# Performance work log

Measured on AMD Instinct MI355X. Metric: run time of the kernel, lower is better.

Reference implementation:

```python
import jax, jax.numpy as jnp
import numpy as np

N_HEADS = 16
DIM = 1024
HEAD_DIM = DIM // N_HEADS

def setup_inputs() -> dict:
    key = jax.random.key(0)
    ks = jax.random.split(key, 5)
    x = jax.random.normal(ks[0], (4, 2048, DIM), dtype=jnp.float32)
    W_attn = jax.random.normal(ks[1], (DIM, 3 * DIM), dtype=jnp.float32) / np.sqrt(DIM)
    b_attn = jnp.zeros((3 * DIM,), dtype=jnp.float32)
    W_proj = jax.random.normal(ks[2], (DIM, DIM), dtype=jnp.float32) / np.sqrt(DIM)
    b_proj = jnp.zeros((DIM,), dtype=jnp.float32)
    return {"x": x, "W_attn": W_attn, "b_attn": b_attn, "W_proj": W_proj, "b_proj": b_proj}

def reference(x, W_attn, b_attn, W_proj, b_proj):
    B, S, D = x.shape
    qkv = x @ W_attn + b_attn                      # [B,S,3D]
    q, k, v = jnp.split(qkv, 3, axis=2)
    def heads(t):
        return t.reshape(B, S, N_HEADS, HEAD_DIM).transpose(0, 2, 1, 3)  # [B,H,S,hd]
    qh, kh, vh = heads(q), heads(k), heads(v)
    scale = 1.0 / np.sqrt(HEAD_DIM).astype(np.float32)
    scores = jnp.einsum('bhqd,bhkd->bhqk', qh, kh) * scale  # [B,H,S,S]
    causal = jnp.tril(jnp.ones((S, S), dtype=bool))
    scores = jnp.where(causal, scores, -jnp.inf)
    probs = jax.nn.softmax(scores, axis=-1)
    ctx = jnp.einsum('bhqk,bhkd->bhqd', probs, vh)           # [B,H,S,hd]
    ctx = ctx.transpose(0, 2, 1, 3).reshape(B, S, D)
    return ctx @ W_proj + b_proj
```

## Files before the change

### kernel.cpp

```cpp
#include <hip/hip_runtime.h>
#include <hip/hip_bf16.h>
#include <stdint.h>

typedef __attribute__((ext_vector_type(4))) float  f32x4a;
typedef __attribute__((ext_vector_type(8))) short  bf16x8s;
typedef __attribute__((ext_vector_type(8))) unsigned short u16x8;

#define QSCALE 0.18033688011112042f

static __device__ __forceinline__ unsigned short f2bf(float f) {
    union { float f; uint32_t u; } v; v.f = f;
    uint32_t u = v.u;
    return (unsigned short)((u + 0x7FFFu + ((u >> 16) & 1u)) >> 16);
}

static __device__ __forceinline__ unsigned int pack2bf(float lo, float hi) {
    __hip_bfloat162 t = __float22bfloat162_rn(make_float2(lo, hi));
    union { __hip_bfloat162 b; unsigned int u; } c; c.b = t;
    return c.u;
}

static __device__ __forceinline__ float exp2a(float x) {
    float r;
    asm("v_exp_f32 %0, %1" : "=v"(r) : "v"(x));
    return r;
}

#define GLL(src, dst)                                                          \
    __builtin_amdgcn_global_load_lds(                                          \
        (const __attribute__((address_space(1))) void*)(src),                  \
        (__attribute__((address_space(3))) void*)(dst), 16, 0, 0)

__global__ __launch_bounds__(256) void k_cvt_bf16(const float* __restrict__ in,
                                                  unsigned short* __restrict__ out, int n8) {
    int i = blockIdx.x * blockDim.x + threadIdx.x;
    if (i >= n8) return;
    const float4* p = (const float4*)(in + (size_t)i * 8);
    float4 a = p[0], b = p[1];
    u16x8 o;
    o[0] = f2bf(a.x); o[1] = f2bf(a.y); o[2] = f2bf(a.z); o[3] = f2bf(a.w);
    o[4] = f2bf(b.x); o[5] = f2bf(b.y); o[6] = f2bf(b.z); o[7] = f2bf(b.w);
    *(u16x8*)(out + (size_t)i * 8) = o;
}

__global__ __launch_bounds__(256) void k_scale_bias(const float* __restrict__ b,
                                                    float* __restrict__ out,
                                                    int n, int nscale, float sc) {
    int i = blockIdx.x * blockDim.x + threadIdx.x;
    if (i >= n) return;
    out[i] = b[i] * (i < nscale ? sc : 1.0f);
}

__global__ __launch_bounds__(256) void k_transpose_w(const float* __restrict__ W,
                                                     unsigned short* __restrict__ Wt,
                                                     int K, int N, float sc, int nscale) {
    __shared__ float tile[64][68];
    int bx = blockIdx.x;
    int ntn = N >> 6;
    int kt = bx / ntn, nt = bx % ntn;
    int t = threadIdx.x;
    int r0 = t >> 4;
    int c4 = (t & 15) << 2;
    for (int i = 0; i < 4; ++i) {
        int k = r0 + i * 16;
        float4 v = *(const float4*)(W + (size_t)(kt * 64 + k) * N + nt * 64 + c4);
        tile[k][c4 + 0] = v.x; tile[k][c4 + 1] = v.y;
        tile[k][c4 + 2] = v.z; tile[k][c4 + 3] = v.w;
    }
    __syncthreads();
    int nl = t >> 2;
    int kc = (t & 3) << 4;
    float s = (nt * 64 + nl < nscale) ? sc : 1.0f;
    unsigned short* dst = Wt + (size_t)(nt * 64 + nl) * K + kt * 64 + kc;
    u16x8 o0, o1;
    for (int i = 0; i < 8; ++i) o0[i] = f2bf(tile[kc + i][nl] * s);
    for (int i = 0; i < 8; ++i) o1[i] = f2bf(tile[kc + 8 + i][nl] * s);
    *(u16x8*)dst = o0;
    *(u16x8*)(dst + 8) = o1;
}

template<int OUT_BF16, int VW>
__global__ __launch_bounds__(512, 2) void k_gemm8p(const unsigned short* __restrict__ A,
                                                   const unsigned short* __restrict__ Bt,
                                                   const float* __restrict__ bias,
                                                   void* __restrict__ Cout,
                                                   unsigned short* __restrict__ vt,
                                                   int M, int N, int K, int ntn) {
    __shared__ __align__(16) unsigned short S[8][8192];
    unsigned short* Sb = &S[0][0];

    int nwg = gridDim.x;
    int bid = blockIdx.x;
    int wg = (bid & 7) * (nwg >> 3) + (bid >> 3);
    int mt = wg / ntn, nt = wg % ntn;
    size_t m0 = (size_t)mt * 256, n0 = (size_t)nt * 256;

    int tid = threadIdx.x;
    int w = tid >> 6, lane = tid & 63;
    int wm = w >> 2, wn = w & 3;
    int l15 = lane & 15, l4 = lane >> 4;

    int srow = tid >> 2;
    int sc = (tid & 3) ^ ((srow >> 1) & 3);
    const unsigned short* Asrc = A  + (m0 + srow) * (size_t)K + sc * 8;
    const unsigned short* Bsrc = Bt + (n0 + srow) * (size_t)K + sc * 8;

#define SLOT(buf, arr, kh) ((((buf) << 2) | ((arr) << 1) | (kh)) * 8192)
#define STAGE(buf, arr, kh, kt)                                                           \
    do {                                                                                  \
        const unsigned short* s_ = ((arr) ? Bsrc : Asrc) + (size_t)(kt) * 64 + (kh) * 32; \
        GLL(s_,                    Sb + SLOT(buf, arr, kh) + tid * 8);                    \
        GLL(s_ + (size_t)128 * K,  Sb + SLOT(buf, arr, kh) + 4096 + tid * 8);             \
    } while (0)

    int ck = (l4 ^ ((l15 >> 1) & 3)) * 8;
    int arowb = wm * 128 + l15;
    int browb = wn * 64 + l15;

#define LD_AF(dst, buf, kh, mh)                                                           \
    _Pragma("unroll")                                                                     \
    for (int q = 0; q < 4; ++q)                                                           \
        dst[q] = *(const bf16x8s*)(Sb + SLOT(buf, 0, kh) + (arowb + (mh) * 64 + q * 16) * 32 + ck);
#define LD_BF(dst, buf, kh)                                                               \
    _Pragma("unroll")                                                                     \
    for (int q = 0; q < 4; ++q)                                                           \
        dst[q] = *(const bf16x8s*)(Sb + SLOT(buf, 1, kh) + (browb + q * 16) * 32 + ck);

    f32x4a acc[8][4] = {};

#define MFMA16(mh, afv, bfv)                                                              \
    do {                                                                                  \
        __builtin_amdgcn_s_setprio(1);                                                    \
        _Pragma("unroll")                                                                 \
        for (int mf = 0; mf < 4; ++mf)                                                    \
            _Pragma("unroll")                                                             \
            for (int nf = 0; nf < 4; ++nf)                                                \
                acc[(mh) * 4 + mf][nf] = __builtin_amdgcn_mfma_f32_16x16x32_bf16(         \
                    afv[mf], bfv[nf], acc[(mh) * 4 + mf][nf], 0, 0, 0);                   \
        __builtin_amdgcn_s_setprio(0);                                                    \
    } while (0)

#define BAR() __builtin_amdgcn_s_barrier()
#define LGKM0()                                                                           \
    do {                                                                                  \
        asm volatile("s_waitcnt lgkmcnt(0)" ::: "memory");                                \
        __builtin_amdgcn_sched_barrier(0);                                                \
    } while (0)

    int NT = K >> 6;

    STAGE(0, 1, 0, 0);
    STAGE(0, 0, 0, 0);
    STAGE(0, 1, 1, 0);
    STAGE(0, 0, 1, 0);
    STAGE(1, 1, 0, 1);
    STAGE(1, 0, 0, 1);
    STAGE(1, 1, 1, 1);
    asm volatile("s_waitcnt vmcnt(6)" ::: "memory");
    __builtin_amdgcn_sched_barrier(0);
    BAR();

    bf16x8s af[4], bf[4], bf2[4];
    for (int t0 = 0; t0 < NT; t0 += 2) {
        int t1 = t0 + 1;
        bool more = (t0 + 2) < NT;
        LD_AF(af, 0, 0, 0);  LD_BF(bf, 0, 0);
        STAGE(1, 0, 1, t1);
        BAR(); LGKM0();
        MFMA16(0, af, bf);
        BAR();
        LD_AF(af, 0, 0, 1);
        if (more) STAGE(0, 1, 0, t0 + 2);
        BAR(); LGKM0();
        MFMA16(1, af, bf);
        BAR();
        LD_AF(af, 0, 1, 0);  LD_BF(bf2, 0, 1);
        if (more) STAGE(0, 0, 0, t0 + 2);
        BAR(); LGKM0();
        MFMA16(0, af, bf2);
        BAR();
        LD_AF(af, 0, 1, 1);
        if (more) STAGE(0, 1, 1, t0 + 2);
        BAR(); LGKM0();
        MFMA16(1, af, bf2);
        if (more) { asm volatile("s_waitcnt vmcnt(6)" ::: "memory"); }
        else      { asm volatile("s_waitcnt vmcnt(0)" ::: "memory"); }
        __builtin_amdgcn_sched_barrier(0);
        BAR();
        LD_AF(af, 1, 0, 0);  LD_BF(bf, 1, 0);
        if (more) STAGE(0, 0, 1, t0 + 2);
        BAR(); LGKM0();
        MFMA16(0, af, bf);
        BAR();
        LD_AF(af, 1, 0, 1);
        if (more) STAGE(1, 1, 0, t1 + 2);
        BAR(); LGKM0();
        MFMA16(1, af, bf);
        BAR();
        LD_AF(af, 1, 1, 0);  LD_BF(bf2, 1, 1);
        if (more) STAGE(1, 0, 0, t1 + 2);
        BAR(); LGKM0();
        MFMA16(0, af, bf2);
        BAR();
        LD_AF(af, 1, 1, 1);
        if (more) STAGE(1, 1, 1, t1 + 2);
        BAR(); LGKM0();
        MFMA16(1, af, bf2);
        if (more) {
            asm volatile("s_waitcnt vmcnt(6)" ::: "memory");
            __builtin_amdgcn_sched_barrier(0);
        }
        BAR();
    }

    if (VW && nt >= 8) {
        int b = (int)(m0 >> 11);
        int sbase = ((int)m0 & 2047) + wm * 128;
        #pragma unroll
        for (int nf = 0; nf < 4; ++nf) {
            int vc = ((int)n0 - 2048) + wn * 64 + nf * 16 + l15;
            int h = vc >> 6, d = vc & 63;
            float bv = bias[2048 + vc];
            unsigned short* vrow = vt + ((size_t)(b * 16 + h) * 64 + d) * 2048;
            #pragma unroll
            for (int mf = 0; mf < 8; ++mf) {
                int s = sbase + mf * 16 + l4 * 4;
                uint2 pv = make_uint2(pack2bf(acc[mf][nf][0] + bv, acc[mf][nf][1] + bv),
                                      pack2bf(acc[mf][nf][2] + bv, acc[mf][nf][3] + bv));
                *(uint2*)(vrow + s) = pv;
            }
        }
    } else {
        #pragma unroll
        for (int nf = 0; nf < 4; ++nf) {
            int col = (int)n0 + wn * 64 + nf * 16 + l15;
            float bv = bias[col];
            #pragma unroll
            for (int mf = 0; mf < 8; ++mf) {
                int rbase = (int)m0 + wm * 128 + mf * 16 + l4 * 4;
                #pragma unroll
                for (int rr = 0; rr < 4; ++rr) {
                    float v = acc[mf][nf][rr] + bv;
                    if (OUT_BF16)
                        ((unsigned short*)Cout)[(size_t)(rbase + rr) * N + col] = f2bf(v);
                    else
                        ((float*)Cout)[(size_t)(rbase + rr) * N + col] = v;
                }
            }
        }
    }
#undef SLOT
#undef STAGE
#undef LD_AF
#undef LD_BF
#undef MFMA16
#undef BAR
#undef LGKM0
}

__global__ __launch_bounds__(256, 4) void k_attn(const unsigned short* __restrict__ qkv,
                                                 const unsigned short* __restrict__ vt,
                                                 unsigned short* __restrict__ ctx) {
    __shared__ unsigned short Ks[2][4096];
    __shared__ unsigned short Vs[2][4096];
    __shared__ unsigned short Pb[4][1024];
    int bx = blockIdx.x;
    int bh = bx & 63;
    int pr = bx >> 6;
    int b = bh >> 4, hd = bh & 15;
    int tid = threadIdx.x;
    int w = tid >> 6, lane = tid & 63;
    int l15 = lane & 15, l4 = lane >> 4;

    const unsigned short* Qb  = qkv + (size_t)b * 2048 * 3072 + hd * 64;
    const unsigned short* Kb  = Qb + 1024;
    const unsigned short* Vtb = vt + (size_t)bh * 64 * 2048;

    int kr0 = tid >> 3, kc0 = tid & 7;
    int kr1 = (tid + 256) >> 3, kc1 = tid & 7;
    const unsigned short* Ksr0 = Kb  + (size_t)kr0 * 3072 + ((kc0 ^ (kr0 & 7)) << 3);
    const unsigned short* Ksr1 = Kb  + (size_t)kr1 * 3072 + ((kc1 ^ (kr1 & 7)) << 3);
    const unsigned short* Vsr0 = Vtb + (size_t)kr0 * 2048 + ((kc0 ^ (kr0 & 7)) << 3);
    const unsigned short* Vsr1 = Vtb + (size_t)kr1 * 2048 + ((kc1 ^ (kr1 & 7)) << 3);
    unsigned short* pbw = &Pb[w][0];

    int prow = l15 * 64;
    int psw  = l15 & 7;
    int ph   = (l4 & 1) * 4;
    int pc0  = ((0 + (l4 >> 1)) ^ psw) * 8;
    int pc1  = ((2 + (l4 >> 1)) ^ psw) * 8;
    int pc2  = ((4 + (l4 >> 1)) ^ psw) * 8;
    int pc3  = ((6 + (l4 >> 1)) ^ psw) * 8;
    int pr0  = ((0 + l4) ^ psw) * 8;
    int pr1  = ((4 + l4) ^ psw) * 8;

#define STAGE(buf, kv0s)                                                                        \
    do {                                                                                        \
        size_t ko_ = (size_t)(kv0s) * 3072;                                                     \
        GLL(Ksr0 + ko_,     &Ks[buf][w * 512]);                                                 \
        GLL(Ksr1 + ko_,     &Ks[buf][2048 + w * 512]);                                          \
        GLL(Vsr0 + (kv0s),  &Vs[buf][w * 512]);                                                 \
        GLL(Vsr1 + (kv0s),  &Vs[buf][2048 + w * 512]);                                          \
    } while (0)

    for (int half = 0; half < 2; ++half) {
        int j = half ? (31 - pr) : pr;
        int q0 = j * 64 + w * 16;
        int qa = q0 + l15;
        bf16x8s qf0, qf1;
        {
            const unsigned short* p = Qb + (size_t)(q0 + l15) * 3072 + l4 * 8;
            qf0 = *(const bf16x8s*)p;
            qf1 = *(const bf16x8s*)(p + 32);
        }
        f32x4a o[4] = {};
        float lrow = 0.0f;
        const int NSTEPS = j + 1;

        STAGE(0, 0);
        __syncthreads();

        int s = 0;
        while (true) {
            int cur = s & 1;
            int kv0 = s << 6;
            if (s + 1 < NSTEPS) STAGE(cur ^ 1, kv0 + 64);

            const unsigned short* Kbuf = Ks[cur];
            const unsigned short* Vbuf = Vs[cur];

            f32x4a z[4];
            __builtin_amdgcn_s_setprio(1);
            #pragma unroll
            for (int f = 0; f < 4; ++f) {
                int rk = f * 16 + l15;
                bf16x8s ka = *(const bf16x8s*)(Kbuf + rk * 64 + ((l4 ^ psw) << 3));
                bf16x8s kb = *(const bf16x8s*)(Kbuf + rk * 64 + (((4 + l4) ^ psw) << 3));
                f32x4a zz = {0.f, 0.f, 0.f, 0.f};
                zz = __builtin_amdgcn_mfma_f32_16x16x32_bf16(ka, qf0, zz, 0, 0, 0);
                zz = __builtin_amdgcn_mfma_f32_16x16x32_bf16(kb, qf1, zz, 0, 0, 0);
                z[f] = zz;
            }
            __builtin_amdgcn_s_setprio(0);

            bf16x8s vf[2][4];
            #pragma unroll
            for (int g = 0; g < 2; ++g)
                #pragma unroll
                for (int nf = 0; nf < 4; ++nf) {
                    int rv = nf * 16 + l15;
                    vf[g][nf] = *(const bf16x8s*)(Vbuf + rv * 64 + (((g * 4 + l4) ^ (rv & 7)) << 3));
                }

            if (s == NSTEPS - 1) {
                #pragma unroll
                for (int f = 0; f < 4; ++f)
                    #pragma unroll
                    for (int r = 0; r < 4; ++r)
                        if (kv0 + f * 16 + l4 * 4 + r > qa) z[f][r] = -1e30f;
            }

            f32x4a p4[4];
            #pragma unroll
            for (int f = 0; f < 4; ++f)
                #pragma unroll
                for (int r = 0; r < 4; ++r)
                    p4[f][r] = exp2a(z[f][r]);

            f32x4a ps = (p4[0] + p4[1]) + (p4[2] + p4[3]);
            float psum = (ps[0] + ps[1]) + (ps[2] + ps[3]);
            psum += __shfl_xor(psum, 16);
            psum += __shfl_xor(psum, 32);
            lrow += psum;

            unsigned int pk[8];
            #pragma unroll
            for (int f = 0; f < 4; ++f) {
                pk[2 * f]     = pack2bf(p4[f][0], p4[f][1]);
                pk[2 * f + 1] = pack2bf(p4[f][2], p4[f][3]);
            }

            *(uint2*)(pbw + prow + pc0 + ph) = make_uint2(pk[0], pk[1]);
            *(uint2*)(pbw + prow + pc1 + ph) = make_uint2(pk[2], pk[3]);
            *(uint2*)(pbw + prow + pc2 + ph) = make_uint2(pk[4], pk[5]);
            *(uint2*)(pbw + prow + pc3 + ph) = make_uint2(pk[6], pk[7]);
            asm volatile("" ::: "memory");
            bf16x8s pa0 = *(const bf16x8s*)(pbw + prow + pr0);
            bf16x8s pa1 = *(const bf16x8s*)(pbw + prow + pr1);
            asm volatile("" ::: "memory");

            __builtin_amdgcn_s_setprio(1);
            #pragma unroll
            for (int nf = 0; nf < 4; ++nf)
                o[nf] = __builtin_amdgcn_mfma_f32_16x16x32_bf16(pa0, vf[0][nf], o[nf], 0, 0, 0);
            #pragma unroll
            for (int nf = 0; nf < 4; ++nf)
                o[nf] = __builtin_amdgcn_mfma_f32_16x16x32_bf16(pa1, vf[1][nf], o[nf], 0, 0, 0);
            __builtin_amdgcn_s_setprio(0);

            ++s;
            if (s == NSTEPS) break;
            __syncthreads();
        }
        __syncthreads();

        float linv[4];
        #pragma unroll
        for (int r = 0; r < 4; ++r) linv[r] = 1.0f / __shfl(lrow, l4 * 4 + r);
        #pragma unroll
        for (int nf = 0; nf < 4; ++nf) {
            int col = hd * 64 + nf * 16 + l15;
            #pragma unroll
            for (int r = 0; r < 4; ++r) {
                int row = q0 + l4 * 4 + r;
                ctx[((size_t)b * 2048 + row) * 1024 + col] = f2bf(o[nf][r] * linv[r]);
            }
        }
    }
#undef STAGE
}

extern "C" void kernel_launch(void* const* d_in, const int* in_sizes, int n_in,
                              void* d_out, int out_size, void* d_ws, size_t ws_size,
                              hipStream_t stream) {
    const float* x      = (const float*)d_in[0];
    const float* W_attn = (const float*)d_in[1];
    const float* b_attn = (const float*)d_in[2];
    const float* W_proj = (const float*)d_in[3];
    const float* b_proj = (const float*)d_in[4];

    char* ws = (char*)d_ws;
    unsigned short* xb  = (unsigned short*)ws; ws += (size_t)8192 * 1024 * 2;
    unsigned short* wta = (unsigned short*)ws; ws += (size_t)3072 * 1024 * 2;
    unsigned short* wtp = (unsigned short*)ws; ws += (size_t)1024 * 1024 * 2;
    unsigned short* qkv = (unsigned short*)ws; ws += (size_t)8192 * 3072 * 2;
    unsigned short* vt  = (unsigned short*)ws; ws += (size_t)64 * 64 * 2048 * 2;
    unsigned short* ctx = (unsigned short*)ws; ws += (size_t)8192 * 1024 * 2;
    float*          sbias = (float*)ws;

    k_cvt_bf16<<<4096, 256, 0, stream>>>(x, xb, 8192 * 1024 / 8);
    k_transpose_w<<<16 * 48, 256, 0, stream>>>(W_attn, wta, 1024, 3072, QSCALE, 1024);
    k_transpose_w<<<16 * 16, 256, 0, stream>>>(W_proj, wtp, 1024, 1024, 1.0f, 0);
    k_scale_bias<<<12, 256, 0, stream>>>(b_attn, sbias, 3072, 1024, QSCALE);
    k_gemm8p<1, 1><<<384, 512, 0, stream>>>(xb, wta, sbias, (void*)qkv, vt, 8192, 3072, 1024, 12);
    k_attn<<<1024, 256, 0, stream>>>(qkv, vt, ctx);
    k_gemm8p<0, 0><<<128, 512, 0, stream>>>(ctx, wtp, b_proj, d_out, nullptr, 8192, 1024, 1024, 4);
}
```

Before: 182.5 us.

## Switch GEMMs to 128x256 tiles with triple-buffered 64-wide K stages

Replaces the 256x256-tile double-buffered GEMM with a 128x256 tile whose K=64 slices sit in a three-slot LDS ring with an 8-chunk XOR swizzle. The grid doubles (768 and 256 workgroups), which gives more waves per CU and better fill across the GPU, especially for the small projection GEMM. Each workgroup now reuses A less per B load and has fewer MFMAs per barrier. LDS use changes to 3*(16K+32K) bytes, which may limit how many workgroups fit per CU.

```diff
diff --git a/kernel.cpp b/kernel.cpp
--- a/kernel.cpp
+++ b/kernel.cpp
@@ -80,63 +80,68 @@
 }
 
 template<int OUT_BF16, int VW>
-__global__ __launch_bounds__(512, 2) void k_gemm8p(const unsigned short* __restrict__ A,
+__global__ __launch_bounds__(512, 2) void k_gemm3b(const unsigned short* __restrict__ A,
                                                    const unsigned short* __restrict__ Bt,
                                                    const float* __restrict__ bias,
                                                    void* __restrict__ Cout,
                                                    unsigned short* __restrict__ vt,
                                                    int M, int N, int K, int ntn) {
-    __shared__ __align__(16) unsigned short S[8][8192];
-    unsigned short* Sb = &S[0][0];
+    __shared__ __align__(16) unsigned short SA[3][8192];
+    __shared__ __align__(16) unsigned short SB[3][16384];
+    unsigned short* SAf = &SA[0][0];
+    unsigned short* SBf = &SB[0][0];
 
     int nwg = gridDim.x;
     int bid = blockIdx.x;
     int wg = (bid & 7) * (nwg >> 3) + (bid >> 3);
     int mt = wg / ntn, nt = wg % ntn;
-    size_t m0 = (size_t)mt * 256, n0 = (size_t)nt * 256;
+    size_t m0 = (size_t)mt * 128, n0 = (size_t)nt * 256;
 
     int tid = threadIdx.x;
     int w = tid >> 6, lane = tid & 63;
     int wm = w >> 2, wn = w & 3;
     int l15 = lane & 15, l4 = lane >> 4;
 
-    int srow = tid >> 2;
-    int sc = (tid & 3) ^ ((srow >> 1) & 3);
-    const unsigned short* Asrc = A  + (m0 + srow) * (size_t)K + sc * 8;
-    const unsigned short* Bsrc = Bt + (n0 + srow) * (size_t)K + sc * 8;
-
-#define SLOT(buf, arr, kh) ((((buf) << 2) | ((arr) << 1) | (kh)) * 8192)
-#define STAGE(buf, arr, kh, kt)                                                           \
+    int srow = tid >> 3;
+    int sch = (tid & 7) ^ (srow & 7);
+    const unsigned short* Asrc = A  + (m0 + srow) * (size_t)K + sch * 8;
+    const unsigned short* Bsrc = Bt + (n0 + srow) * (size_t)K + sch * 8;
+
+#define STG_A(bufi, kt)                                                                   \
     do {                                                                                  \
-        const unsigned short* s_ = ((arr) ? Bsrc : Asrc) + (size_t)(kt) * 64 + (kh) * 32; \
-        GLL(s_,                    Sb + SLOT(buf, arr, kh) + tid * 8);                    \
-        GLL(s_ + (size_t)128 * K,  Sb + SLOT(buf, arr, kh) + 4096 + tid * 8);             \
+        GLL(Asrc + (size_t)(kt) * 64,                    SAf + (bufi) * 8192 + tid * 8);  \
+        GLL(Asrc + (size_t)(kt) * 64 + (size_t)64 * K,   SAf + (bufi) * 8192 + 4096 + tid * 8); \
     } while (0)
-
-    int ck = (l4 ^ ((l15 >> 1) & 3)) * 8;
-    int arowb = wm * 128 + l15;
-    int browb = wn * 64 + l15;
-
-#define LD_AF(dst, buf, kh, mh)                                                           \
-    _Pragma("unroll")                                                                     \
-    for (int q = 0; q < 4; ++q)                                                           \
-        dst[q] = *(const bf16x8s*)(Sb + SLOT(buf, 0, kh) + (arowb + (mh) * 64 + q * 16) * 32 + ck);
-#define LD_BF(dst, buf, kh)                                                               \
-    _Pragma("unroll")                                                                     \
-    for (int q = 0; q < 4; ++q)                                                           \
-        dst[q] = *(const bf16x8s*)(Sb + SLOT(buf, 1, kh) + (browb + q * 16) * 32 + ck);
-
-    f32x4a acc[8][4] = {};
-
-#define MFMA16(mh, afv, bfv)                                                              \
+#define STG_B(bufi, kt, i)                                                                \
+    GLL(Bsrc + (size_t)(kt) * 64 + (size_t)(64 * (i)) * K,                                \
+        SBf + (bufi) * 16384 + (i) * 4096 + tid * 8)
+
+    int ck0 = ((l4)     ^ (l15 & 7)) * 8;
+    int ck1 = ((l4 + 4) ^ (l15 & 7)) * 8;
+    int arow = wm * 64 + l15;
+    int brow = wn * 64 + l15;
+
+#define LD_FR(bufi, ck)                                                                   \
+    do {                                                                                  \
+        _Pragma("unroll")                                                                 \
+        for (int q = 0; q < 4; ++q)                                                       \
+            af[q] = *(const bf16x8s*)(SAf + (bufi) * 8192  + (arow + q * 16) * 64 + (ck)); \
+        _Pragma("unroll")                                                                 \
+        for (int q = 0; q < 4; ++q)                                                       \
+            bf[q] = *(const bf16x8s*)(SBf + (bufi) * 16384 + (brow + q * 16) * 64 + (ck)); \
+    } while (0)
+
+    f32x4a acc[4][4] = {};
+
+#define MFMA16()                                                                          \
     do {                                                                                  \
         __builtin_amdgcn_s_setprio(1);                                                    \
         _Pragma("unroll")                                                                 \
         for (int mf = 0; mf < 4; ++mf)                                                    \
             _Pragma("unroll")                                                             \
             for (int nf = 0; nf < 4; ++nf)                                                \
-                acc[(mh) * 4 + mf][nf] = __builtin_amdgcn_mfma_f32_16x16x32_bf16(         \
-                    afv[mf], bfv[nf], acc[(mh) * 4 + mf][nf], 0, 0, 0);                   \
+                acc[mf][nf] = __builtin_amdgcn_mfma_f32_16x16x32_bf16(                    \
+                    af[mf], bf[nf], acc[mf][nf], 0, 0, 0);                                \
         __builtin_amdgcn_s_setprio(0);                                                    \
     } while (0)
 
@@ -149,73 +154,36 @@
 
     int NT = K >> 6;
 
-    STAGE(0, 1, 0, 0);
-    STAGE(0, 0, 0, 0);
-    STAGE(0, 1, 1, 0);
-    STAGE(0, 0, 1, 0);
-    STAGE(1, 1, 0, 1);
-    STAGE(1, 0, 0, 1);
-    STAGE(1, 1, 1, 1);
+    STG_A(0, 0); STG_B(0, 0, 0); STG_B(0, 0, 1); STG_B(0, 0, 2); STG_B(0, 0, 3);
+    STG_A(1, 1); STG_B(1, 1, 0); STG_B(1, 1, 1); STG_B(1, 1, 2); STG_B(1, 1, 3);
     asm volatile("s_waitcnt vmcnt(6)" ::: "memory");
     __builtin_amdgcn_sched_barrier(0);
     BAR();
 
-    bf16x8s af[4], bf[4], bf2[4];
-    for (int t0 = 0; t0 < NT; t0 += 2) {
-        int t1 = t0 + 1;
-        bool more = (t0 + 2) < NT;
-        LD_AF(af, 0, 0, 0);  LD_BF(bf, 0, 0);
-        STAGE(1, 0, 1, t1);
+    bf16x8s af[4], bf[4];
+    int cur = 0;
+    for (int t = 0; t < NT; ++t) {
+        int stg = cur + 2; if (stg >= 3) stg -= 3;
+        bool more = (t + 2) < NT;
+        LD_FR(cur, ck0);
+        if (more) { STG_A(stg, t + 2); STG_B(stg, t + 2, 0); }
         BAR(); LGKM0();
-        MFMA16(0, af, bf);
+        MFMA16();
         BAR();
-        LD_AF(af, 0, 0, 1);
-        if (more) STAGE(0, 1, 0, t0 + 2);
+        LD_FR(cur, ck1);
+        if (more) { STG_B(stg, t + 2, 1); STG_B(stg, t + 2, 2); STG_B(stg, t + 2, 3); }
         BAR(); LGKM0();
-        MFMA16(1, af, bf);
-        BAR();
-        LD_AF(af, 0, 1, 0);  LD_BF(bf2, 0, 1);
-        if (more) STAGE(0, 0, 0, t0 + 2);
-        BAR(); LGKM0();
-        MFMA16(0, af, bf2);
-        BAR();
-        LD_AF(af, 0, 1, 1);
-        if (more) STAGE(0, 1, 1, t0 + 2);
-        BAR(); LGKM0();
-        MFMA16(1, af, bf2);
-        if (more) { asm volatile("s_waitcnt vmcnt(6)" ::: "memory"); }
-        else      { asm volatile("s_waitcnt vmcnt(0)" ::: "memory"); }
+        MFMA16();
+        if (t < NT - 2)       { asm volatile("s_waitcnt vmcnt(6)" ::: "memory"); }
+        else if (t == NT - 2) { asm volatile("s_waitcnt vmcnt(0)" ::: "memory"); }
         __builtin_amdgcn_sched_barrier(0);
         BAR();
-        LD_AF(af, 1, 0, 0);  LD_BF(bf, 1, 0);
-        if (more) STAGE(0, 0, 1, t0 + 2);
-        BAR(); LGKM0();
-        MFMA16(0, af, bf);
-        BAR();
-        LD_AF(af, 1, 0, 1);
-        if (more) STAGE(1, 1, 0, t1 + 2);
-        BAR(); LGKM0();
-        MFMA16(1, af, bf);
-        BAR();
-        LD_AF(af, 1, 1, 0);  LD_BF(bf2, 1, 1);
-        if (more) STAGE(1, 0, 0, t1 + 2);
-        BAR(); LGKM0();
-        MFMA16(0, af, bf2);
-        BAR();
-        LD_AF(af, 1, 1, 1);
-        if (more) STAGE(1, 1, 1, t1 + 2);
-        BAR(); LGKM0();
-        MFMA16(1, af, bf2);
-        if (more) {
-            asm volatile("s_waitcnt vmcnt(6)" ::: "memory");
-            __builtin_amdgcn_sched_barrier(0);
-        }
-        BAR();
+        cur = (cur + 1 == 3) ? 0 : cur + 1;
     }
 
     if (VW && nt >= 8) {
         int b = (int)(m0 >> 11);
-        int sbase = ((int)m0 & 2047) + wm * 128;
+        int sb_ = ((int)m0 & 2047) + wm * 64;
         #pragma unroll
         for (int nf = 0; nf < 4; ++nf) {
             int vc = ((int)n0 - 2048) + wn * 64 + nf * 16 + l15;
@@ -223,8 +191,8 @@
             float bv = bias[2048 + vc];
             unsigned short* vrow = vt + ((size_t)(b * 16 + h) * 64 + d) * 2048;
             #pragma unroll
-            for (int mf = 0; mf < 8; ++mf) {
-                int s = sbase + mf * 16 + l4 * 4;
+            for (int mf = 0; mf < 4; ++mf) {
+                int s = sb_ + mf * 16 + l4 * 4;
                 uint2 pv = make_uint2(pack2bf(acc[mf][nf][0] + bv, acc[mf][nf][1] + bv),
                                       pack2bf(acc[mf][nf][2] + bv, acc[mf][nf][3] + bv));
                 *(uint2*)(vrow + s) = pv;
@@ -236,8 +204,8 @@
             int col = (int)n0 + wn * 64 + nf * 16 + l15;
             float bv = bias[col];
             #pragma unroll
-            for (int mf = 0; mf < 8; ++mf) {
-                int rbase = (int)m0 + wm * 128 + mf * 16 + l4 * 4;
+            for (int mf = 0; mf < 4; ++mf) {
+                int rbase = (int)m0 + wm * 64 + mf * 16 + l4 * 4;
                 #pragma unroll
                 for (int rr = 0; rr < 4; ++rr) {
                     float v = acc[mf][nf][rr] + bv;
@@ -249,10 +217,9 @@
             }
         }
     }
-#undef SLOT
-#undef STAGE
-#undef LD_AF
-#undef LD_BF
+#undef STG_A
+#undef STG_B
+#undef LD_FR
 #undef MFMA16
 #undef BAR
 #undef LGKM0
@@ -442,7 +409,7 @@
     k_transpose_w<<<16 * 48, 256, 0, stream>>>(W_attn, wta, 1024, 3072, QSCALE, 1024);
     k_transpose_w<<<16 * 16, 256, 0, stream>>>(W_proj, wtp, 1024, 1024, 1.0f, 0);
     k_scale_bias<<<12, 256, 0, stream>>>(b_attn, sbias, 3072, 1024, QSCALE);
-    k_gemm8p<1, 1><<<384, 512, 0, stream>>>(xb, wta, sbias, (void*)qkv, vt, 8192, 3072, 1024, 12);
+    k_gemm3b<1, 1><<<768, 512, 0, stream>>>(xb, wta, sbias, (void*)qkv, vt, 8192, 3072, 1024, 12);
     k_attn<<<1024, 256, 0, stream>>>(qkv, vt, ctx);
-    k_gemm8p<0, 0><<<128, 512, 0, stream>>>(ctx, wtp, b_proj, d_out, nullptr, 8192, 1024, 1024, 4);
-}
+    k_gemm3b<0, 0><<<256, 512, 0, stream>>>(ctx, wtp, b_proj, d_out, nullptr, 8192, 1024, 1024, 4);
+}
```

Result: faster. 168.6 us (-7.6%).
